# Optimization experiments

Measured on AMD Instinct MI355X. Metric: run time of the kernel, lower is better.

## Reference

```python
import jax, jax.numpy as jnp
import numpy as np

N_HEAD = 12
N_EMBD = 768

def setup_inputs() -> dict:
    key = jax.random.key(0)
    k1, k2, k3 = jax.random.split(key, 3)
    B, T, C = 4, 2048, N_EMBD
    x = jax.random.normal(k1, (B, T, C), dtype=jnp.float32)
    w_attn = jax.random.normal(k2, (C, 3 * C), dtype=jnp.float32) * (C ** -0.5)
    b_attn = jnp.zeros((3 * C,), dtype=jnp.float32)
    w_proj = jax.random.normal(k3, (C, C), dtype=jnp.float32) * (C ** -0.5)
    b_proj = jnp.zeros((C,), dtype=jnp.float32)
    return {"x": x, "w_attn": w_attn, "b_attn": b_attn, "w_proj": w_proj, "b_proj": b_proj}

def reference(x, w_attn, b_attn, w_proj, b_proj):
    B, T, C = x.shape
    H = N_HEAD
    D = C // H
    qkv = x @ w_attn + b_attn  # [B,T,3C]
    q, k, v = jnp.split(qkv, 3, axis=-1)
    # [B,H,T,D]
    q = q.reshape(B, T, H, D).transpose(0, 2, 1, 3)
    k = k.reshape(B, T, H, D).transpose(0, 2, 1, 3)
    v = v.reshape(B, T, H, D).transpose(0, 2, 1, 3)
    # NOTE: source scales by n_embd**-0.5, not head_dim**-0.5
    scores = jnp.einsum('bhqd,bhkd->bhqk', q, k) * (C ** -0.5)
    causal = jnp.triu(jnp.ones((T, T), dtype=bool), k=1)  # True above diagonal
    scores = jnp.where(causal, -jnp.inf, scores)
    attn = jax.nn.softmax(scores, axis=-1)
    out = jnp.einsum('bhqk,bhkd->bhqd', attn, v)  # [B,H,T,D]
    out = out.transpose(0, 2, 1, 3).reshape(B, T, C)
    return out @ w_proj + b_proj
```

## Files before the change

kernel.cpp:

```cpp
#include <hip/hip_runtime.h>
#include <cstdint>
#include <cstddef>

typedef __attribute__((ext_vector_type(8))) short bf8_t;
typedef __attribute__((ext_vector_type(4))) float f4_t;
typedef __attribute__((ext_vector_type(16))) float f16v_t;
typedef __attribute__((ext_vector_type(2))) unsigned u2_t;
typedef __attribute__((ext_vector_type(4))) unsigned u4_t;

#define DEVFN static __device__ __forceinline__
#define MFMA16(a, b, c) __builtin_amdgcn_mfma_f32_16x16x32_bf16(a, b, c, 0, 0, 0)
#define MFMA32(a, b, c) __builtin_amdgcn_mfma_f32_32x32x16_bf16(a, b, c, 0, 0, 0)

constexpr float kQscale = 0.05205877317700523f;

DEVFN short f2bs(float f) {
  uint32_t u = __builtin_bit_cast(uint32_t, f);
  u = (u + 0x7FFFu + ((u >> 16) & 1u)) >> 16;
  return (short)(uint16_t)u;
}

DEVFN unsigned cvtpk(float lo, float hi) {
  unsigned r;
  asm("v_cvt_pk_bf16_f32 %0, %1, %2" : "=v"(r) : "v"(lo), "v"(hi));
  return r;
}

DEVFN float red2_sum(float v) { return v + __shfl_xor(v, 32, 64); }

DEVFN void gload16(const void* g, void* l) {
  __builtin_amdgcn_global_load_lds(
      (const __attribute__((address_space(1))) void*)g,
      (__attribute__((address_space(3))) void*)l, 16, 0, 0);
}

__global__ __launch_bounds__(256) void prep(const float* __restrict__ x,
                                            short* __restrict__ xb,
                                            const float* __restrict__ w_attn,
                                            short* __restrict__ wat,
                                            const float* __restrict__ w_proj,
                                            short* __restrict__ wpt) {
  __shared__ float tile[32][33];
  const int blk = blockIdx.x, tid = threadIdx.x;
  if (blk < 3072) {
    const int i = blk * 256 + tid;
    const f4_t* p = (const f4_t*)x + (size_t)i * 2;
    f4_t a = p[0], b = p[1];
    bf8_t h;
    h[0] = f2bs(a[0]); h[1] = f2bs(a[1]); h[2] = f2bs(a[2]); h[3] = f2bs(a[3]);
    h[4] = f2bs(b[0]); h[5] = f2bs(b[1]); h[6] = f2bs(b[2]); h[7] = f2bs(b[3]);
    *((bf8_t*)xb + i) = h;
    return;
  }
  const float* w;
  short* wT;
  int N, n0, k0;
  if (blk < 4800) {
    const int bb = blk - 3072;
    w = w_attn; wT = wat; N = 2304;
    n0 = (bb % 72) << 5; k0 = (bb / 72) << 5;
  } else {
    const int bb = blk - 4800;
    w = w_proj; wT = wpt; N = 768;
    n0 = (bb % 24) << 5; k0 = (bb / 24) << 5;
  }
  const int tx = tid & 31, ty = tid >> 5;
#pragma unroll
  for (int i = 0; i < 4; ++i)
    tile[ty * 4 + i][tx] = w[(size_t)(k0 + ty * 4 + i) * N + n0 + tx];
  __syncthreads();
#pragma unroll
  for (int i = 0; i < 4; ++i)
    wT[(size_t)(n0 + ty * 4 + i) * 768 + k0 + tx] = f2bs(tile[tx][ty * 4 + i]);
}

template <int EPI, int BN, int NW>
__global__ __launch_bounds__(NW * 64) void gemm_bf16(
    const short* __restrict__ A, const short* __restrict__ Bt,
    const float* __restrict__ bias, float* __restrict__ outF,
    short* __restrict__ qb, short* __restrict__ kb, short* __restrict__ vtb,
    int Mdim, int Ndim, int Kdim) {
  constexpr int NT = NW * 64;
  constexpr int WCN = NW / 2;
  constexpr int WNW = BN / WCN;
  constexpr int NI = WNW / 16;
  constexpr int ACH = 16 / NW;
  constexpr int BCH = BN / (8 * NW);
  __shared__ char smem[32768 + 2 * (BN << 7)];
  const int nbx = gridDim.x;
  const int bid = blockIdx.x + nbx * blockIdx.y;
  const int xcd = bid & 7, slot = bid >> 3;
  const int mp = xcd + ((slot / nbx) << 3);
  const int np = slot % nbx;
  const int m0 = mp << 7, n0 = np * BN;
  const int tid = threadIdx.x;
  const int lane = tid & 63, wid = tid >> 6;
  const int wr = wid / WCN, wc = wid % WCN;
  const int g = lane >> 4, cl = lane & 15;
  const int ldb = Kdim << 1;

  f4_t acc[4][NI];
#pragma unroll
  for (int mi = 0; mi < 4; ++mi)
#pragma unroll
    for (int ni = 0; ni < NI; ++ni) acc[mi][ni] = (f4_t){0.f, 0.f, 0.f, 0.f};

  const char* ga = (const char*)(A + (size_t)m0 * Kdim);
  const char* gb = (const char*)(Bt + (size_t)n0 * Kdim);
  auto stage = [&](int b, int ks) {
    const int k0b = ks << 7;
    char* Ab = smem + (b << 14);
    char* Bb = smem + 32768 + b * (BN << 7);
#pragma unroll
    for (int i = 0; i < ACH; ++i) {
      const int doff = (wid * ACH + i) << 10;
      const int boff = doff + lane * 16;
      const int row = boff >> 7;
      const int src = row * ldb + k0b + ((boff & 127) ^ ((row & 7) << 4));
      gload16(ga + src, Ab + doff);
    }
#pragma unroll
    for (int i = 0; i < BCH; ++i) {
      const int doff = (wid * BCH + i) << 10;
      const int boff = doff + lane * 16;
      const int row = boff >> 7;
      const int src = row * ldb + k0b + ((boff & 127) ^ ((row & 7) << 4));
      gload16(gb + src, Bb + doff);
    }
  };

  const int nk = Kdim >> 6;
  stage(0, 0);
  __syncthreads();

  int cur = 0;
  for (int ks = 0; ks < nk; ++ks) {
    const int ksn = (ks + 1 < nk) ? ks + 1 : ks;
    stage(cur ^ 1, ksn);
    const char* Ab = smem + (cur << 14);
    const char* Bb = smem + 32768 + cur * (BN << 7);
#pragma unroll
    for (int kk = 0; kk < 2; ++kk) {
      bf8_t af[4], bfv[NI];
#pragma unroll
      for (int mi = 0; mi < 4; ++mi) {
        int lrow = (wr << 6) + (mi << 4) + cl;
        af[mi] = *(const bf8_t*)&Ab[(lrow << 7) + ((((kk << 2) + g) ^ (lrow & 7)) << 4)];
      }
#pragma unroll
      for (int ni = 0; ni < NI; ++ni) {
        int lrow = wc * WNW + (ni << 4) + cl;
        bfv[ni] = *(const bf8_t*)&Bb[(lrow << 7) + ((((kk << 2) + g) ^ (lrow & 7)) << 4)];
      }
#pragma unroll
      for (int mi = 0; mi < 4; ++mi)
#pragma unroll
        for (int ni = 0; ni < NI; ++ni)
          acc[mi][ni] = MFMA16(af[mi], bfv[ni], acc[mi][ni]);
    }
    __syncthreads();
    cur ^= 1;
  }

  if constexpr (EPI == 1) {
#pragma unroll
    for (int ni = 0; ni < NI; ++ni) {
      const int n = n0 + wc * WNW + (ni << 4) + cl;
      const float bv = bias[n];
#pragma unroll
      for (int mi = 0; mi < 4; ++mi)
#pragma unroll
        for (int r = 0; r < 4; ++r) {
          const int m = m0 + (wr << 6) + (mi << 4) + (g << 2) + r;
          outF[(size_t)m * 768 + n] = acc[mi][ni][r] + bv;
        }
    }
  } else {
    short* T = (short*)smem;
    const int sec = n0 / 768;
    const float qs = (sec == 0) ? kQscale : 1.0f;
#pragma unroll
    for (int ni = 0; ni < NI; ++ni) {
      const int colT = wc * WNW + (ni << 4) + cl;
      const float bv = bias[n0 + colT];
#pragma unroll
      for (int mi = 0; mi < 4; ++mi)
#pragma unroll
        for (int r = 0; r < 4; ++r) {
          const int row = (wr << 6) + (mi << 4) + (g << 2) + r;
          T[row * 132 + colT] = f2bs((acc[mi][ni][r] + bv) * qs);
        }
    }
    __syncthreads();
    if (sec < 2) {
      short* dst0 = (sec == 0) ? qb : kb;
      const int tl = tid & 127;
      const int hh2 = (tid >> 7) & 1;
      const int half = tid >> 8;
      constexpr int JN = (NT == 256) ? 8 : 4;
      const int m = m0 + tl, b = m >> 11, t = m & 2047;
      const int hh = ((n0 - sec * 768) >> 6) + hh2;
      short* dst = dst0 + (size_t)(b * 12 + hh) * 131072 + (size_t)t * 64 + half * 32;
      const short* src = T + tl * 132 + hh2 * 64 + half * 32;
#pragma unroll
      for (int j = 0; j < JN; ++j)
        *(bf8_t*)(dst + j * 8) = *(const bf8_t*)(src + j * 8);
    } else {
      const int chunk = tid & 15;
      constexpr int DLS = NT >> 4;
      const int m = m0 + (chunk << 3);
      const int b = m >> 11, t = m & 2047;
#pragma unroll
      for (int c8 = 0; c8 < 128 / DLS; ++c8) {
        const int dl = (tid >> 4) + c8 * DLS;
        const int nloc = n0 - 1536 + dl;
        const int hh = nloc >> 6, d = nloc & 63;
        bf8_t tmp;
#pragma unroll
        for (int j = 0; j < 8; ++j)
          tmp[j] = T[((chunk << 3) + j) * 132 + dl];
        *(bf8_t*)(vtb + (size_t)(b * 12 + hh) * 131072 + (size_t)d * 2048 + t) = tmp;
      }
    }
  }
}

__global__ __launch_bounds__(256, 2) void attn_fwd(const short* __restrict__ Q,
                                                   const short* __restrict__ K,
                                                   const short* __restrict__ Vt,
                                                   short* __restrict__ O) {
  __shared__ char kv[32768];
  const int tid = threadIdx.x;
  const int lane = tid & 63, wid = tid >> 6;
  const int blk = blockIdx.x;
  const int bh = blk % 48;
  const int qg = 15 - blk / 48;
  const int qt = (qg << 2) + wid;
  const int q0 = qt << 5;
  const int col = lane & 31, hi = lane >> 5;

  const short* Qb = Q + (size_t)bh * 131072;
  const short* Kb = K + (size_t)bh * 131072;
  const short* Vb = Vt + (size_t)bh * 131072;

  bf8_t qf[4];
#pragma unroll
  for (int dc = 0; dc < 4; ++dc)
    qf[dc] = *(const bf8_t*)(Qb + (size_t)(q0 + col) * 64 + dc * 16 + hi * 8);

  const f16v_t zf = {0.f,0.f,0.f,0.f,0.f,0.f,0.f,0.f,0.f,0.f,0.f,0.f,0.f,0.f,0.f,0.f};
  f16v_t o0 = zf, o1 = zf;
  float ls[4] = {0.f, 0.f, 0.f, 0.f};

  const int nt = qg + 1;
  const int kxor = (col & 7) << 4;

  u4_t stg[8];
  auto load_regs = [&](int kcs) {
    if (wid < 2) {
      const char* g = (const char*)(Kb + (size_t)kcs * 64);
#pragma unroll
      for (int i = 0; i < 8; ++i)
        stg[i] = *(const u4_t*)(g + (wid << 13) + (i << 10) + lane * 16);
    } else {
      const char* g = (const char*)Vb + (size_t)kcs * 2;
#pragma unroll
      for (int i = 0; i < 8; ++i) {
        const int boff = ((wid - 2) << 13) + (i << 10) + lane * 16;
        const int row = boff >> 8;
        stg[i] = *(const u4_t*)(g + row * 4096 + (boff & 255));
      }
    }
  };
  auto write_lds = [&]() {
    if (wid < 2) {
#pragma unroll
      for (int i = 0; i < 8; ++i) {
        const int boff = (wid << 13) + (i << 10) + lane * 16;
        *(u4_t*)(kv + (boff ^ (((boff >> 7) & 7) << 4))) = stg[i];
      }
    } else {
#pragma unroll
      for (int i = 0; i < 8; ++i) {
        const int boff = ((wid - 2) << 13) + (i << 10) + lane * 16;
        const int row = boff >> 8;
        *(u4_t*)(kv + 16384 + (boff & ~255) + ((boff & 255) ^ ((row & 7) << 4))) = stg[i];
      }
    }
  };

  load_regs(0);
  write_lds();
  __syncthreads();

  for (int st = 0; st < nt; ++st) {
    const bool more = (st + 1 < nt);
    if (more) load_regs((st + 1) << 7);

#pragma unroll
    for (int h = 0; h < 2; ++h) {
      const int kc = (st << 7) + (h << 6);
      if (kc < q0 + 32) {
        const char* Kl = kv + (h << 13);
        const char* Vl = kv + 16384;
        f16v_t s0 = zf, s1 = zf;
#pragma unroll
        for (int dc = 0; dc < 4; ++dc) {
          const int fo = (dc * 32 + hi * 16) ^ kxor;
          bf8_t k0 = *(const bf8_t*)(Kl + col * 128 + fo);
          bf8_t k1 = *(const bf8_t*)(Kl + (32 + col) * 128 + fo);
          __builtin_amdgcn_s_setprio(1);
          s0 = MFMA32(k0, qf[dc], s0);
          s1 = MFMA32(k1, qf[dc], s1);
          __builtin_amdgcn_s_setprio(0);
        }
        if (kc + 63 > q0) {
          const int qq = q0 + col;
#pragma unroll
          for (int r = 0; r < 16; ++r) {
            const int kb_ = kc + (r & 3) + 8 * (r >> 2) + 4 * hi;
            if (kb_ > qq) s0[r] = -1e30f;
            if (kb_ + 32 > qq) s1[r] = -1e30f;
          }
        }
#pragma unroll
        for (int r = 0; r < 16; ++r) {
          s0[r] = __builtin_amdgcn_exp2f(s0[r]);
          s1[r] = __builtin_amdgcn_exp2f(s1[r]);
        }
#pragma unroll
        for (int r = 0; r < 4; ++r)
          ls[r] += ((s0[r] + s0[r + 4]) + (s0[r + 8] + s0[r + 12])) +
                   ((s1[r] + s1[r + 4]) + (s1[r + 8] + s1[r + 12]));
#pragma unroll
        for (int c = 0; c < 4; ++c) {
          const int b8 = (c & 1) * 8;
          float p0, p1, p2, p3, p4, p5, p6, p7;
          if (c < 2) {
            p0 = s0[b8+0]; p1 = s0[b8+1]; p2 = s0[b8+2]; p3 = s0[b8+3];
            p4 = s0[b8+4]; p5 = s0[b8+5]; p6 = s0[b8+6]; p7 = s0[b8+7];
          } else {
            p0 = s1[b8+0]; p1 = s1[b8+1]; p2 = s1[b8+2]; p3 = s1[b8+3];
            p4 = s1[b8+4]; p5 = s1[b8+5]; p6 = s1[b8+6]; p7 = s1[b8+7];
          }
          unsigned w0 = cvtpk(p0, p1), w1 = cvtpk(p2, p3);
          unsigned w2 = cvtpk(p4, p5), w3 = cvtpk(p6, p7);
          unsigned x0 = (unsigned)__shfl_xor((int)w0, 32, 64);
          unsigned x1 = (unsigned)__shfl_xor((int)w1, 32, 64);
          unsigned x2 = (unsigned)__shfl_xor((int)w2, 32, 64);
          unsigned x3 = (unsigned)__shfl_xor((int)w3, 32, 64);
          unsigned T0 = hi ? x2 : w0;
          unsigned T1 = hi ? x3 : w1;
          unsigned T2 = hi ? w2 : x0;
          unsigned T3 = hi ? w3 : x1;
          const bf8_t pf = __builtin_bit_cast(bf8_t, (u4_t){T0, T1, T2, T3});
          const int vo = ((h << 7) + c * 32 + hi * 16) ^ kxor;
          bf8_t v0 = *(const bf8_t*)(Vl + col * 256 + vo);
          bf8_t v1 = *(const bf8_t*)(Vl + (32 + col) * 256 + vo);
          __builtin_amdgcn_s_setprio(1);
          o0 = MFMA32(v0, pf, o0);
          o1 = MFMA32(v1, pf, o1);
          __builtin_amdgcn_s_setprio(0);
        }
      }
    }
    if (more) {
      __syncthreads();
      write_lds();
      __syncthreads();
    }
  }

  const float l = red2_sum((ls[0] + ls[1]) + (ls[2] + ls[3]));
  const float rl = 1.0f / l;
  const int b_ = bh / 12, hh = bh % 12;
  short* Op = O + (size_t)b_ * 2048 * 768 + (size_t)(q0 + col) * 768 + hh * 64;
#pragma unroll
  for (int rq = 0; rq < 4; ++rq) {
    u2_t w0, w1;
    w0[0] = cvtpk(o0[4*rq+0] * rl, o0[4*rq+1] * rl);
    w0[1] = cvtpk(o0[4*rq+2] * rl, o0[4*rq+3] * rl);
    w1[0] = cvtpk(o1[4*rq+0] * rl, o1[4*rq+1] * rl);
    w1[1] = cvtpk(o1[4*rq+2] * rl, o1[4*rq+3] * rl);
    *(u2_t*)(Op + rq * 8 + hi * 4) = w0;
    *(u2_t*)(Op + 32 + rq * 8 + hi * 4) = w1;
  }
}

extern "C" void kernel_launch(void* const* d_in, const int* in_sizes, int n_in,
                              void* d_out, int out_size, void* d_ws, size_t ws_size,
                              hipStream_t stream) {
  const float* x      = (const float*)d_in[0];
  const float* w_attn = (const float*)d_in[1];
  const float* b_attn = (const float*)d_in[2];
  const float* w_proj = (const float*)d_in[3];
  const float* b_proj = (const float*)d_in[4];
  float* out = (float*)d_out;

  const size_t QSZ = (size_t)4 * 12 * 2048 * 64;
  short* ws  = (short*)d_ws;
  short* qb  = ws;
  short* kb  = qb + QSZ;
  short* vtb = kb + QSZ;
  short* xb  = vtb + QSZ;
  short* ob  = xb;
  short* wat = xb + QSZ;
  short* wpt = wat + (size_t)2304 * 768;

  prep<<<5376, 256, 0, stream>>>(x, xb, w_attn, wat, w_proj, wpt);

  gemm_bf16<0, 128, 8><<<dim3(18, 64), 512, 0, stream>>>(xb, wat, b_attn, nullptr,
                                                         qb, kb, vtb, 8192, 2304, 768);
  attn_fwd<<<768, 256, 0, stream>>>(qb, kb, vtb, ob);
  gemm_bf16<1, 64, 4><<<dim3(12, 64), 256, 0, stream>>>(ob, wpt, b_proj, out,
                                                        nullptr, nullptr, nullptr, 8192, 768, 768);
}
```

Baseline: 129.2 us.

## Double-buffer attention K/V tiles with direct global-to-LDS loads and permlane swap

Replaces the register-staged K/V prefetch with double-buffered LDS tiles filled through direct global-to-LDS loads (gload16). The swizzle moves from the LDS store address to the global source address, and each iteration now needs one barrier instead of two. This frees the staging registers, and the next tile's load overlaps compute on the current buffer. The P-fragment cross-half exchange also switches from four shfl_xor plus selects to two permlane32_swap ops. In exchange, LDS use doubles to 64KB per block, which may limit occupancy, and the last iteration issues a redundant clamped load.

After: 123.9 us. 4.1% less time.

```diff
diff --git a/kernel.cpp b/kernel.cpp
--- a/kernel.cpp
+++ b/kernel.cpp
@@ -229,7 +229,7 @@
                                                    const short* __restrict__ K,
                                                    const short* __restrict__ Vt,
                                                    short* __restrict__ O) {
-  __shared__ char kv[32768];
+  __shared__ char kv_lds[2][32768];
   const int tid = threadIdx.x;
   const int lane = tid & 63, wid = tid >> 6;
   const int blk = blockIdx.x;
@@ -255,54 +255,45 @@
   const int nt = qg + 1;
   const int kxor = (col & 7) << 4;
 
-  u4_t stg[8];
-  auto load_regs = [&](int kcs) {
+  auto stage = [&](int b, int kcs) {
+    char* buf = &kv_lds[b][0];
     if (wid < 2) {
       const char* g = (const char*)(Kb + (size_t)kcs * 64);
 #pragma unroll
-      for (int i = 0; i < 8; ++i)
-        stg[i] = *(const u4_t*)(g + (wid << 13) + (i << 10) + lane * 16);
+      for (int i = 0; i < 8; ++i) {
+        const int doff = (wid << 13) + (i << 10);
+        const int boff = doff + lane * 16;
+        const int src = boff ^ (((boff >> 7) & 7) << 4);
+        gload16(g + src, buf + doff);
+      }
     } else {
       const char* g = (const char*)Vb + (size_t)kcs * 2;
 #pragma unroll
       for (int i = 0; i < 8; ++i) {
-        const int boff = ((wid - 2) << 13) + (i << 10) + lane * 16;
+        const int doff = ((wid - 2) << 13) + (i << 10);
+        const int boff = doff + lane * 16;
         const int row = boff >> 8;
-        stg[i] = *(const u4_t*)(g + row * 4096 + (boff & 255));
+        const int src = row * 4096 + ((boff & 255) ^ ((row & 7) << 4));
+        gload16(g + src, buf + 16384 + doff);
       }
     }
   };
-  auto write_lds = [&]() {
-    if (wid < 2) {
-#pragma unroll
-      for (int i = 0; i < 8; ++i) {
-        const int boff = (wid << 13) + (i << 10) + lane * 16;
-        *(u4_t*)(kv + (boff ^ (((boff >> 7) & 7) << 4))) = stg[i];
-      }
-    } else {
-#pragma unroll
-      for (int i = 0; i < 8; ++i) {
-        const int boff = ((wid - 2) << 13) + (i << 10) + lane * 16;
-        const int row = boff >> 8;
-        *(u4_t*)(kv + 16384 + (boff & ~255) + ((boff & 255) ^ ((row & 7) << 4))) = stg[i];
-      }
-    }
-  };
-
-  load_regs(0);
-  write_lds();
+
+  stage(0, 0);
   __syncthreads();
 
+  int cur = 0;
   for (int st = 0; st < nt; ++st) {
-    const bool more = (st + 1 < nt);
-    if (more) load_regs((st + 1) << 7);
+    int kcn = (st + 1) << 7;
+    if (kcn > 1920) kcn = 1920;
+    stage(cur ^ 1, kcn);
 
 #pragma unroll
     for (int h = 0; h < 2; ++h) {
       const int kc = (st << 7) + (h << 6);
       if (kc < q0 + 32) {
-        const char* Kl = kv + (h << 13);
-        const char* Vl = kv + 16384;
+        const char* Kl = &kv_lds[cur][h << 13];
+        const char* Vl = &kv_lds[cur][16384];
         f16v_t s0 = zf, s1 = zf;
 #pragma unroll
         for (int dc = 0; dc < 4; ++dc) {
@@ -345,15 +336,9 @@
           }
           unsigned w0 = cvtpk(p0, p1), w1 = cvtpk(p2, p3);
           unsigned w2 = cvtpk(p4, p5), w3 = cvtpk(p6, p7);
-          unsigned x0 = (unsigned)__shfl_xor((int)w0, 32, 64);
-          unsigned x1 = (unsigned)__shfl_xor((int)w1, 32, 64);
-          unsigned x2 = (unsigned)__shfl_xor((int)w2, 32, 64);
-          unsigned x3 = (unsigned)__shfl_xor((int)w3, 32, 64);
-          unsigned T0 = hi ? x2 : w0;
-          unsigned T1 = hi ? x3 : w1;
-          unsigned T2 = hi ? w2 : x0;
-          unsigned T3 = hi ? w3 : x1;
-          const bf8_t pf = __builtin_bit_cast(bf8_t, (u4_t){T0, T1, T2, T3});
+          u2_t ra = __builtin_amdgcn_permlane32_swap(w0, w2, false, false);
+          u2_t rb = __builtin_amdgcn_permlane32_swap(w1, w3, false, false);
+          const bf8_t pf = __builtin_bit_cast(bf8_t, (u4_t){ra[0], rb[0], ra[1], rb[1]});
           const int vo = ((h << 7) + c * 32 + hi * 16) ^ kxor;
           bf8_t v0 = *(const bf8_t*)(Vl + col * 256 + vo);
           bf8_t v1 = *(const bf8_t*)(Vl + (32 + col) * 256 + vo);
@@ -364,11 +349,8 @@
         }
       }
     }
-    if (more) {
-      __syncthreads();
-      write_lds();
-      __syncthreads();
-    }
+    __syncthreads();
+    cur ^= 1;
   }
 
   const float l = red2_sum((ls[0] + ls[1]) + (ls[2] + ls[3]));
```
